# Kernel optimization log

Measured on AMD Instinct MI355X. Metric: run time of the kernel, lower is better.

## Reference

```python
import jax, jax.numpy as jnp
import numpy as np

N_NODES = 100000


def gcn_conv(x, src, dst, W, b, n):
    # x: [N, F_in]; src/dst: [E+N] (self-loops already appended)
    h = x @ W  # [N, F_out]
    deg = jax.ops.segment_sum(jnp.ones_like(dst, dtype=h.dtype), dst, num_segments=n)
    dinv = jnp.where(deg > 0, jax.lax.rsqrt(deg), 0.0)
    norm = dinv[src] * dinv[dst]  # [E+N]
    msgs = h[src] * norm[:, None]  # gather + scale
    out = jax.ops.segment_sum(msgs, dst, num_segments=n)  # scatter-add at dst
    return out + b


def setup_inputs() -> dict:
    key = jax.random.key(0)
    k1, k2, k3, ke = jax.random.split(key, 4)
    d = 64
    x = jax.random.normal(k1, (N_NODES, d), dtype=jnp.float32)
    edge_index = jax.random.randint(ke, (2, 1000000), 0, N_NODES, dtype=jnp.int64)
    s = 1.0 / np.sqrt(d)
    W1 = jax.random.normal(k2, (d, d), dtype=jnp.float32) * s
    b1 = jnp.zeros((d,), dtype=jnp.float32)
    W2 = jax.random.normal(k3, (d, d), dtype=jnp.float32) * s
    b2 = jnp.zeros((d,), dtype=jnp.float32)
    return {"x": x, "edge_index": edge_index, "W1": W1, "b1": b1, "W2": W2, "b2": b2}


def reference(x, edge_index, W1, b1, W2, b2):
    n = x.shape[0]
    loops = jnp.arange(n, dtype=edge_index.dtype)
    src = jnp.concatenate([edge_index[0], loops])
    dst = jnp.concatenate([edge_index[1], loops])
    h = gcn_conv(x, src, dst, W1, b1, n)
    h = jax.nn.relu(h)
    out = gcn_conv(h, src, dst, W2, b2, n)
    return out
```

## Files before the change

kernel.cpp:

```cpp
#include <hip/hip_runtime.h>

#define F 64
#define NCH 256

typedef __attribute__((ext_vector_type(8))) short bf16x8;
typedef __attribute__((ext_vector_type(4))) float f32x4;

static __device__ __forceinline__ unsigned short f2bf(float f) {
    unsigned u = __float_as_uint(f);
    return (unsigned short)((u + 0x7fffu + ((u >> 16) & 1u)) >> 16);
}
static __device__ __forceinline__ float bflo(unsigned u) { return __uint_as_float(u << 16); }
static __device__ __forceinline__ float bfhi(unsigned u) { return __uint_as_float(u & 0xffff0000u); }

__global__ __launch_bounds__(256) void k_fused0(const int* __restrict__ dst,
                                                int* __restrict__ histM,
                                                const float* __restrict__ W1,
                                                const float* __restrict__ W2,
                                                unsigned short* __restrict__ W2t,
                                                const float* __restrict__ X,
                                                unsigned short* __restrict__ hs1,
                                                int E, int chunk, int NB, int N) {
    __shared__ int h[512];
    __shared__ unsigned short Wl[64 * 72];
    __shared__ unsigned short Xs[64 * 72];
    const int t = threadIdx.x;
    const int b = blockIdx.x;

    if (b < NCH) {
        for (int i = t; i < NB; i += 256) h[i] = 0;
        __syncthreads();
        const int lo = b * chunk;
        const int hi = min(E, lo + chunk);
        for (int e = lo + t; e < hi; e += 256) {
            atomicAdd(&h[dst[e] >> 8], 1);
        }
        __syncthreads();
        for (int i = t; i < NB; i += 256) histM[i * NCH + b] = h[i];
        return;
    }
    if (b == NCH) {
#pragma unroll
        for (int i = 0; i < 16; ++i) {
            int e = t + i * 256;
            int n = e >> 6, k = e & 63;
            W2t[e] = f2bf(W2[k * 64 + n]);
        }
        return;
    }

    const int row0 = (b - NCH - 1) * 64;
#pragma unroll
    for (int i = 0; i < 16; ++i) {
        int e = t + i * 256;
        int n = e >> 6, k = e & 63;
        Wl[n * 72 + k] = f2bf(W1[k * 64 + n]);
    }
#pragma unroll
    for (int i = 0; i < 4; ++i) {
        int idx = t + i * 256;
        int r = idx >> 4, c = (idx & 15) * 4;
        int gr = row0 + r;
        float4 v = make_float4(0.f, 0.f, 0.f, 0.f);
        if (gr < N) v = *(const float4*)&X[(size_t)gr * F + c];
        unsigned p0 = (unsigned)f2bf(v.x) | ((unsigned)f2bf(v.y) << 16);
        unsigned p1 = (unsigned)f2bf(v.z) | ((unsigned)f2bf(v.w) << 16);
        *(uint2*)&Xs[r * 72 + c] = make_uint2(p0, p1);
    }
    __syncthreads();

    const int w    = t >> 6;
    const int lane = t & 63;
    const int l15  = lane & 15;
    const int quad = lane >> 4;

    bf16x8 bf[4][2];
#pragma unroll
    for (int ct = 0; ct < 4; ++ct)
#pragma unroll
        for (int kc = 0; kc < 2; ++kc)
            bf[ct][kc] = *(const bf16x8*)&Wl[(ct * 16 + l15) * 72 + kc * 32 + quad * 8];

    const int am = w * 16 + l15;
    bf16x8 af0 = *(const bf16x8*)&Xs[am * 72 + quad * 8];
    bf16x8 af1 = *(const bf16x8*)&Xs[am * 72 + 32 + quad * 8];

    f32x4 acc[4];
#pragma unroll
    for (int ct = 0; ct < 4; ++ct) {
        f32x4 z = {0.f, 0.f, 0.f, 0.f};
        z = __builtin_amdgcn_mfma_f32_16x16x32_bf16(af0, bf[ct][0], z, 0, 0, 0);
        z = __builtin_amdgcn_mfma_f32_16x16x32_bf16(af1, bf[ct][1], z, 0, 0, 0);
        acc[ct] = z;
    }

#pragma unroll
    for (int ct = 0; ct < 4; ++ct) {
#pragma unroll
        for (int r = 0; r < 4; ++r) {
            int row = row0 + w * 16 + quad * 4 + r;
            if (row < N)
                hs1[(size_t)row * F + ct * 16 + l15] = f2bf(acc[ct][r]);
        }
    }
}

__global__ __launch_bounds__(256) void s_part(const int* __restrict__ v,
                                              int* __restrict__ part, int M) {
    __shared__ int sd[256];
    const int t = threadIdx.x;
    const int base = blockIdx.x * 1024 + t * 4;
    int s = 0;
    if (base + 3 < M) {
        int4 d = *(const int4*)&v[base];
        s = d.x + d.y + d.z + d.w;
    } else {
#pragma unroll
        for (int j = 0; j < 4; ++j) if (base + j < M) s += v[base + j];
    }
    sd[t] = s;
    __syncthreads();
    for (int off = 128; off > 0; off >>= 1) {
        if (t < off) sd[t] += sd[t + off];
        __syncthreads();
    }
    if (t == 0) part[blockIdx.x] = sd[0];
}

__global__ __launch_bounds__(256) void s_scanp(int* __restrict__ part, int nb) {
    __shared__ int sums[256];
    const int t = threadIdx.x;
    int s = (t < nb) ? part[t] : 0;
    sums[t] = s;
    __syncthreads();
    for (int off = 1; off < 256; off <<= 1) {
        int v = (t >= off) ? sums[t - off] : 0;
        __syncthreads();
        sums[t] += v;
        __syncthreads();
    }
    if (t < nb) part[t] = sums[t] - s;
}

__global__ __launch_bounds__(256) void s_emit(int* __restrict__ v,
                                              const int* __restrict__ part, int M) {
    __shared__ int sums[256];
    const int t = threadIdx.x;
    const int base = blockIdx.x * 1024 + t * 4;
    int d0 = 0, d1 = 0, d2 = 0, d3 = 0;
    if (base + 3 < M) {
        int4 d = *(const int4*)&v[base];
        d0 = d.x; d1 = d.y; d2 = d.z; d3 = d.w;
    } else {
        if (base + 0 < M) d0 = v[base + 0];
        if (base + 1 < M) d1 = v[base + 1];
        if (base + 2 < M) d2 = v[base + 2];
        if (base + 3 < M) d3 = v[base + 3];
    }
    int tot = d0 + d1 + d2 + d3;
    sums[t] = tot;
    __syncthreads();
    for (int off = 1; off < 256; off <<= 1) {
        int x = (t >= off) ? sums[t - off] : 0;
        __syncthreads();
        sums[t] += x;
        __syncthreads();
    }
    int o0 = part[blockIdx.x] + sums[t] - tot;
    int e0 = o0, e1 = o0 + d0, e2 = e1 + d1, e3 = e2 + d2;
    if (base + 3 < M) {
        *(int4*)&v[base] = make_int4(e0, e1, e2, e3);
    } else {
        int ee[4] = {e0, e1, e2, e3};
        for (int j = 0; j < 4; ++j) if (base + j < M) v[base + j] = ee[j];
    }
}

__global__ __launch_bounds__(256) void k_scatter2(const int* __restrict__ src,
                                                  const int* __restrict__ dst,
                                                  const int* __restrict__ scanM,
                                                  int* __restrict__ ebuf,
                                                  int E, int chunk, int NB) {
    extern __shared__ int cur[];
    const int t = threadIdx.x;
    for (int i = t; i < NB; i += 256) cur[i] = scanM[i * NCH + blockIdx.x];
    __syncthreads();
    const int lo = blockIdx.x * chunk;
    const int hi = min(E, lo + chunk);
    for (int e = lo + t; e < hi; e += 256) {
        int s = src[e];
        int d = dst[e];
        int p = atomicAdd(&cur[d >> 8], 1);
        ebuf[p] = s | ((d & 255) << 17);
    }
}

__global__ __launch_bounds__(256) void k_csr(const int* __restrict__ ebuf,
                                             const int* __restrict__ scanM,
                                             int* __restrict__ rowptr,
                                             int* __restrict__ csr,
                                             float* __restrict__ dinv,
                                             int N, int E, int NB) {
    __shared__ int hist[256];
    __shared__ int scn[256];
    __shared__ int cur[256];
    const int t = threadIdx.x;
    const int bkt = blockIdx.x;
    const int beg = scanM[bkt * NCH];
    const int end = (bkt + 1 < NB) ? scanM[(bkt + 1) * NCH] : E;

    hist[t] = 0;
    __syncthreads();
    for (int e = beg + t; e < end; e += 256)
        atomicAdd(&hist[((unsigned)ebuf[e]) >> 17], 1);
    __syncthreads();

    scn[t] = hist[t];
    __syncthreads();
    for (int off = 1; off < 256; off <<= 1) {
        int v = (t >= off) ? scn[t - off] : 0;
        __syncthreads();
        scn[t] += v;
        __syncthreads();
    }

    {
        int excl = scn[t] - hist[t];
        int rp = beg + excl;
        int node = (bkt << 8) + t;
        cur[t] = rp;
        if (node < N) {
            rowptr[node] = rp;
            dinv[node] = rsqrtf((float)(hist[t] + 1));
        }
    }
    if (bkt == NB - 1 && t == 0) rowptr[N] = E;
    __syncthreads();

    for (int e = beg + t; e < end; e += 256) {
        int pk = ebuf[e];
        int p = atomicAdd(&cur[((unsigned)pk) >> 17], 1);
        csr[p] = pk & 0x1FFFF;
    }
}

__global__ __launch_bounds__(512) void k_aggmm(const unsigned short* __restrict__ hs1,
                                               const int* __restrict__ rowptr,
                                               const int* __restrict__ csr,
                                               const unsigned short* __restrict__ W2t,
                                               const float* __restrict__ b1,
                                               const float* __restrict__ dinv,
                                               unsigned short* __restrict__ hs2, int N) {
    __shared__ unsigned short Act[256 * 72];
    __shared__ unsigned short Wl[64 * 72];
    __shared__ float sdv[256];
    const int t = threadIdx.x;
    const int node0 = blockIdx.x << 8;

    {
        int idx = t;
        int n = idx >> 3, k = (idx & 7) * 8;
        *(uint4*)&Wl[n * 72 + k] = ((const uint4*)W2t)[idx];
    }

    const int lane = t & 7;
    const int nsub = t >> 3;
    const uint4* hsb = (const uint4*)hs1;
    float4 bb0 = *(const float4*)&b1[lane * 8];
    float4 bb1 = *(const float4*)&b1[lane * 8 + 4];

#pragma unroll
    for (int it = 0; it < 4; ++it) {
        int local = it * 64 + nsub;
        int node = node0 + local;
        float sc = 0.f;
        unsigned p0 = 0, p1 = 0, p2 = 0, p3 = 0;
        if (node < N) {
            int beg = rowptr[node];
            int end = rowptr[node + 1];
            sc = rsqrtf((float)(end - beg + 1));
            float a0, a1, a2, a3, a4, a5, a6, a7;
            {
                uint4 u = hsb[(size_t)node * 8 + lane];
                a0 = sc * bflo(u.x); a1 = sc * bfhi(u.x);
                a2 = sc * bflo(u.y); a3 = sc * bfhi(u.y);
                a4 = sc * bflo(u.z); a5 = sc * bfhi(u.z);
                a6 = sc * bflo(u.w); a7 = sc * bfhi(u.w);
            }
            for (int base = beg; base < end; base += 16) {
                int i0 = base + lane;
                int i1 = base + 8 + lane;
                int x0 = (i0 < end) ? csr[i0] : 0;
                int x1 = (i1 < end) ? csr[i1] : 0;
                uint4 r[16];
                float dv[16];
#pragma unroll
                for (int k = 0; k < 8; ++k) {
                    int s = __shfl(x0, k, 8);
                    r[k] = hsb[(size_t)s * 8 + lane];
                    dv[k] = dinv[s];
                }
#pragma unroll
                for (int k = 0; k < 8; ++k) {
                    int s = __shfl(x1, k, 8);
                    r[8 + k] = hsb[(size_t)s * 8 + lane];
                    dv[8 + k] = dinv[s];
                }
                int cnt = min(16, end - base);
#pragma unroll
                for (int k = 0; k < 16; ++k) {
                    if (k < cnt) {
                        uint4 u = r[k];
                        float w = dv[k];
                        a0 = fmaf(bflo(u.x), w, a0); a1 = fmaf(bfhi(u.x), w, a1);
                        a2 = fmaf(bflo(u.y), w, a2); a3 = fmaf(bfhi(u.y), w, a3);
                        a4 = fmaf(bflo(u.z), w, a4); a5 = fmaf(bfhi(u.z), w, a5);
                        a6 = fmaf(bflo(u.w), w, a6); a7 = fmaf(bfhi(u.w), w, a7);
                    }
                }
            }
            float o0 = fmaxf(a0 * sc + bb0.x, 0.f), o1 = fmaxf(a1 * sc + bb0.y, 0.f);
            float o2 = fmaxf(a2 * sc + bb0.z, 0.f), o3 = fmaxf(a3 * sc + bb0.w, 0.f);
            float o4 = fmaxf(a4 * sc + bb1.x, 0.f), o5 = fmaxf(a5 * sc + bb1.y, 0.f);
            float o6 = fmaxf(a6 * sc + bb1.z, 0.f), o7 = fmaxf(a7 * sc + bb1.w, 0.f);
            p0 = (unsigned)f2bf(o0) | ((unsigned)f2bf(o1) << 16);
            p1 = (unsigned)f2bf(o2) | ((unsigned)f2bf(o3) << 16);
            p2 = (unsigned)f2bf(o4) | ((unsigned)f2bf(o5) << 16);
            p3 = (unsigned)f2bf(o6) | ((unsigned)f2bf(o7) << 16);
        }
        *(uint4*)&Act[local * 72 + lane * 8] = make_uint4(p0, p1, p2, p3);
        if (lane == 0) sdv[local] = sc;
    }
    __syncthreads();

    const int w    = t >> 6;
    const int l    = t & 63;
    const int l15  = l & 15;
    const int quad = l >> 4;

    bf16x8 bf[4][2];
#pragma unroll
    for (int nt = 0; nt < 4; ++nt)
#pragma unroll
        for (int kc = 0; kc < 2; ++kc)
            bf[nt][kc] = *(const bf16x8*)&Wl[(nt * 16 + l15) * 72 + kc * 32 + quad * 8];

#pragma unroll
    for (int mt = 0; mt < 2; ++mt) {
        int m0 = w * 32 + mt * 16;
        bf16x8 af0 = *(const bf16x8*)&Act[(m0 + l15) * 72 + quad * 8];
        bf16x8 af1 = *(const bf16x8*)&Act[(m0 + l15) * 72 + 32 + quad * 8];
#pragma unroll
        for (int nt = 0; nt < 4; ++nt) {
            f32x4 z = {0.f, 0.f, 0.f, 0.f};
            z = __builtin_amdgcn_mfma_f32_16x16x32_bf16(af0, bf[nt][0], z, 0, 0, 0);
            z = __builtin_amdgcn_mfma_f32_16x16x32_bf16(af1, bf[nt][1], z, 0, 0, 0);
#pragma unroll
            for (int r = 0; r < 4; ++r) {
                int row = m0 + quad * 4 + r;
                int node = node0 + row;
                if (node < N)
                    hs2[((size_t)nt * N + node) * 16 + l15] = f2bf(z[r] * sdv[row]);
            }
        }
    }
}

__global__ __launch_bounds__(256) void k_agg2(const unsigned short* __restrict__ hs2,
                                              const int* __restrict__ rowptr,
                                              const int* __restrict__ csr,
                                              const float* __restrict__ dinv,
                                              const float* __restrict__ b,
                                              float* __restrict__ out, int N) {
    const int slice = blockIdx.x & 3;
    const int chunk = blockIdx.x >> 2;
    const int t = threadIdx.x;
    const int node = chunk * 64 + (t >> 2);
    const int lane = t & 3;
    if (node >= N) return;
    const int beg = rowptr[node];
    const int end = rowptr[node + 1];
    const unsigned short* hp = hs2 + (size_t)slice * N * 16;

    float a[16];
#pragma unroll
    for (int j = 0; j < 16; ++j) a[j] = 0.f;

    int e = beg + lane;
    int i0 = (e < end) ? csr[e] : -1;
    int i1 = (e + 4 < end) ? csr[e + 4] : -1;
    while (i0 >= 0) {
        int i2 = (e + 8  < end) ? csr[e + 8]  : -1;
        int i3 = (e + 12 < end) ? csr[e + 12] : -1;
        {
            const uint4* p = (const uint4*)(hp + (size_t)i0 * 16);
            uint4 u0 = p[0];
            uint4 u1 = p[1];
            a[0] += bflo(u0.x); a[1] += bfhi(u0.x);
            a[2] += bflo(u0.y); a[3] += bfhi(u0.y);
            a[4] += bflo(u0.z); a[5] += bfhi(u0.z);
            a[6] += bflo(u0.w); a[7] += bfhi(u0.w);
            a[8]  += bflo(u1.x); a[9]  += bfhi(u1.x);
            a[10] += bflo(u1.y); a[11] += bfhi(u1.y);
            a[12] += bflo(u1.z); a[13] += bfhi(u1.z);
            a[14] += bflo(u1.w); a[15] += bfhi(u1.w);
        }
        if (i1 >= 0) {
            const uint4* p = (const uint4*)(hp + (size_t)i1 * 16);
            uint4 u0 = p[0];
            uint4 u1 = p[1];
            a[0] += bflo(u0.x); a[1] += bfhi(u0.x);
            a[2] += bflo(u0.y); a[3] += bfhi(u0.y);
            a[4] += bflo(u0.z); a[5] += bfhi(u0.z);
            a[6] += bflo(u0.w); a[7] += bfhi(u0.w);
            a[8]  += bflo(u1.x); a[9]  += bfhi(u1.x);
            a[10] += bflo(u1.y); a[11] += bfhi(u1.y);
            a[12] += bflo(u1.z); a[13] += bfhi(u1.z);
            a[14] += bflo(u1.w); a[15] += bfhi(u1.w);
        }
        i0 = i2;
        i1 = i3;
        e += 8;
    }

    float h[8];
#pragma unroll
    for (int k = 0; k < 8; ++k) {
        float lo = a[k]     + __shfl_xor(a[k], 2, 4);
        float hi = a[k + 8] + __shfl_xor(a[k + 8], 2, 4);
        h[k] = (lane & 2) ? hi : lo;
    }
    float v[4];
#pragma unroll
    for (int k = 0; k < 4; ++k) {
        float lo = h[k]     + __shfl_xor(h[k], 1, 4);
        float hi = h[k + 4] + __shfl_xor(h[k + 4], 1, 4);
        v[k] = (lane & 1) ? hi : lo;
    }

    const float sc = dinv[node];
    const int j0 = lane * 4;
    uint2 sv = *(const uint2*)(hp + (size_t)node * 16 + j0);
    float s0 = bflo(sv.x), s1 = bfhi(sv.x), s2 = bflo(sv.y), s3 = bfhi(sv.y);
    float4 bb = *(const float4*)&b[slice * 16 + j0];
    float4 o = make_float4((v[0] + s0) * sc + bb.x,
                           (v[1] + s1) * sc + bb.y,
                           (v[2] + s2) * sc + bb.z,
                           (v[3] + s3) * sc + bb.w);
    *(float4*)&out[(size_t)node * F + slice * 16 + j0] = o;
}

extern "C" void kernel_launch(void* const* d_in, const int* in_sizes, int n_in,
                              void* d_out, int out_size, void* d_ws, size_t ws_size,
                              hipStream_t stream) {
    const float* x  = (const float*)d_in[0];
    const int*   ei = (const int*)d_in[1];
    const float* W1 = (const float*)d_in[2];
    const float* b1 = (const float*)d_in[3];
    const float* W2 = (const float*)d_in[4];
    const float* b2 = (const float*)d_in[5];
    float* out = (float*)d_out;

    const int N = in_sizes[0] / F;
    const int E = in_sizes[1] / 2;
    const int* src = ei;
    const int* dst = ei + E;

    const int NB = (N + 255) >> 8;
    const int chunk = (E + NCH - 1) / NCH;
    const int M  = NB * NCH;
    const int Mp = ((M + 1023) / 1024) * 1024;
    const int nb2 = Mp / 1024;

    char* ws = (char*)d_ws;
    size_t a = 0;
    unsigned short* W2t = (unsigned short*)(ws + a); a += (4096 * 2 + 255) & ~(size_t)255;
    float* dinv   = (float*)(ws + a); a += ((size_t)N * 4 + 255) & ~(size_t)255;
    int*   part2  = (int*)(ws + a);   a += ((size_t)nb2 * 4 + 255) & ~(size_t)255;
    int*   rowptr = (int*)(ws + a);   a += ((size_t)(N + 1) * 4 + 255) & ~(size_t)255;
    int*   histM  = (int*)(ws + a);   a += ((size_t)Mp * 4 + 255) & ~(size_t)255;
    int*   ebuf   = (int*)(ws + a);   a += ((size_t)E * 4 + 255) & ~(size_t)255;
    int*   csr    = (int*)(ws + a);   a += ((size_t)E * 4 + 255) & ~(size_t)255;
    unsigned short* hs1 = (unsigned short*)(ws + a); a += ((size_t)N * F * 2 + 255) & ~(size_t)255;
    unsigned short* hs2 = (unsigned short*)(ws + a);

    const size_t ldsNB = (size_t)NB * 4;
    const int gGemm = (N + 63) / 64;
    const int gAgg2 = ((N + 63) / 64) * 4;

    k_fused0<<<NCH + 1 + gGemm, 256, 0, stream>>>(dst, histM, W1, W2, W2t, x, hs1,
                                                  E, chunk, NB, N);
    s_part<<<nb2, 256, 0, stream>>>(histM, part2, M);
    s_scanp<<<1, 256, 0, stream>>>(part2, nb2);
    s_emit<<<nb2, 256, 0, stream>>>(histM, part2, M);
    k_scatter2<<<NCH, 256, ldsNB, stream>>>(src, dst, histM, ebuf, E, chunk, NB);
    k_csr<<<NB, 256, 0, stream>>>(ebuf, histM, rowptr, csr, dinv, N, E, NB);

    k_aggmm<<<NB, 512, 0, stream>>>(hs1, rowptr, csr, W2t, b1, dinv, hs2, N);
    k_agg2<<<gAgg2, 256, 0, stream>>>(hs2, rowptr, csr, dinv, b2, out, N);
}
```

Before: 193.4 us.

## Pre-scale layer-1 features by dinv in CSR kernel and fold scan launch

Source-side normalization is now applied once per node: k_csr multiplies each hs1 row by its dinv and writes it back in bf16. k_aggmm then drops the per-edge dinv gather and multiply and just sums neighbor rows. The standalone partial-scan kernel is also removed, and each emit block reduces the preceding partials itself, saving one launch. The cost is an extra read-modify-write of hs1 plus one more bf16 rounding of the scaled features.

```diff
diff --git a/kernel.cpp b/kernel.cpp
--- a/kernel.cpp
+++ b/kernel.cpp
@@ -127,26 +127,22 @@
     if (t == 0) part[blockIdx.x] = sd[0];
 }
 
-__global__ __launch_bounds__(256) void s_scanp(int* __restrict__ part, int nb) {
+__global__ __launch_bounds__(256) void s_emit2(int* __restrict__ v,
+                                               const int* __restrict__ part, int M) {
     __shared__ int sums[256];
-    const int t = threadIdx.x;
-    int s = (t < nb) ? part[t] : 0;
-    sums[t] = s;
-    __syncthreads();
-    for (int off = 1; off < 256; off <<= 1) {
-        int v = (t >= off) ? sums[t - off] : 0;
-        __syncthreads();
-        sums[t] += v;
-        __syncthreads();
-    }
-    if (t < nb) part[t] = sums[t] - s;
-}
-
-__global__ __launch_bounds__(256) void s_emit(int* __restrict__ v,
-                                              const int* __restrict__ part, int M) {
-    __shared__ int sums[256];
-    const int t = threadIdx.x;
-    const int base = blockIdx.x * 1024 + t * 4;
+    __shared__ int red[256];
+    const int t = threadIdx.x;
+    const int b = blockIdx.x;
+
+    red[t] = (t < b) ? part[t] : 0;
+    __syncthreads();
+    for (int off = 128; off > 0; off >>= 1) {
+        if (t < off) red[t] += red[t + off];
+        __syncthreads();
+    }
+    const int pref = red[0];
+
+    const int base = b * 1024 + t * 4;
     int d0 = 0, d1 = 0, d2 = 0, d3 = 0;
     if (base + 3 < M) {
         int4 d = *(const int4*)&v[base];
@@ -166,7 +162,7 @@
         sums[t] += x;
         __syncthreads();
     }
-    int o0 = part[blockIdx.x] + sums[t] - tot;
+    int o0 = pref + sums[t] - tot;
     int e0 = o0, e1 = o0 + d0, e2 = e1 + d1, e3 = e2 + d2;
     if (base + 3 < M) {
         *(int4*)&v[base] = make_int4(e0, e1, e2, e3);
@@ -200,6 +196,7 @@
                                              int* __restrict__ rowptr,
                                              int* __restrict__ csr,
                                              float* __restrict__ dinv,
+                                             unsigned short* __restrict__ hs1,
                                              int N, int E, int NB) {
     __shared__ int hist[256];
     __shared__ int scn[256];
@@ -224,17 +221,32 @@
         __syncthreads();
     }
 
+    const int node = (bkt << 8) + t;
+    float sc = 0.f;
     {
         int excl = scn[t] - hist[t];
         int rp = beg + excl;
-        int node = (bkt << 8) + t;
         cur[t] = rp;
         if (node < N) {
             rowptr[node] = rp;
-            dinv[node] = rsqrtf((float)(hist[t] + 1));
+            sc = rsqrtf((float)(hist[t] + 1));
+            dinv[node] = sc;
         }
     }
     if (bkt == NB - 1 && t == 0) rowptr[N] = E;
+
+    if (node < N) {
+        uint4* rowp = (uint4*)(hs1 + (size_t)node * F);
+#pragma unroll
+        for (int j = 0; j < 8; ++j) {
+            uint4 u = rowp[j];
+            u.x = (unsigned)f2bf(bflo(u.x) * sc) | ((unsigned)f2bf(bfhi(u.x) * sc) << 16);
+            u.y = (unsigned)f2bf(bflo(u.y) * sc) | ((unsigned)f2bf(bfhi(u.y) * sc) << 16);
+            u.z = (unsigned)f2bf(bflo(u.z) * sc) | ((unsigned)f2bf(bfhi(u.z) * sc) << 16);
+            u.w = (unsigned)f2bf(bflo(u.w) * sc) | ((unsigned)f2bf(bfhi(u.w) * sc) << 16);
+            rowp[j] = u;
+        }
+    }
     __syncthreads();
 
     for (int e = beg + t; e < end; e += 256) {
@@ -249,7 +261,6 @@
                                                const int* __restrict__ csr,
                                                const unsigned short* __restrict__ W2t,
                                                const float* __restrict__ b1,
-                                               const float* __restrict__ dinv,
                                                unsigned short* __restrict__ hs2, int N) {
     __shared__ unsigned short Act[256 * 72];
     __shared__ unsigned short Wl[64 * 72];
@@ -282,10 +293,10 @@
             float a0, a1, a2, a3, a4, a5, a6, a7;
             {
                 uint4 u = hsb[(size_t)node * 8 + lane];
-                a0 = sc * bflo(u.x); a1 = sc * bfhi(u.x);
-                a2 = sc * bflo(u.y); a3 = sc * bfhi(u.y);
-                a4 = sc * bflo(u.z); a5 = sc * bfhi(u.z);
-                a6 = sc * bflo(u.w); a7 = sc * bfhi(u.w);
+                a0 = bflo(u.x); a1 = bfhi(u.x);
+                a2 = bflo(u.y); a3 = bfhi(u.y);
+                a4 = bflo(u.z); a5 = bfhi(u.z);
+                a6 = bflo(u.w); a7 = bfhi(u.w);
             }
             for (int base = beg; base < end; base += 16) {
                 int i0 = base + lane;
@@ -293,29 +304,25 @@
                 int x0 = (i0 < end) ? csr[i0] : 0;
                 int x1 = (i1 < end) ? csr[i1] : 0;
                 uint4 r[16];
-                float dv[16];
 #pragma unroll
                 for (int k = 0; k < 8; ++k) {
                     int s = __shfl(x0, k, 8);
                     r[k] = hsb[(size_t)s * 8 + lane];
-                    dv[k] = dinv[s];
                 }
 #pragma unroll
                 for (int k = 0; k < 8; ++k) {
                     int s = __shfl(x1, k, 8);
                     r[8 + k] = hsb[(size_t)s * 8 + lane];
-                    dv[8 + k] = dinv[s];
                 }
                 int cnt = min(16, end - base);
 #pragma unroll
                 for (int k = 0; k < 16; ++k) {
                     if (k < cnt) {
                         uint4 u = r[k];
-                        float w = dv[k];
-                        a0 = fmaf(bflo(u.x), w, a0); a1 = fmaf(bfhi(u.x), w, a1);
-                        a2 = fmaf(bflo(u.y), w, a2); a3 = fmaf(bfhi(u.y), w, a3);
-                        a4 = fmaf(bflo(u.z), w, a4); a5 = fmaf(bfhi(u.z), w, a5);
-                        a6 = fmaf(bflo(u.w), w, a6); a7 = fmaf(bfhi(u.w), w, a7);
+                        a0 += bflo(u.x); a1 += bfhi(u.x);
+                        a2 += bflo(u.y); a3 += bfhi(u.y);
+                        a4 += bflo(u.z); a5 += bfhi(u.z);
+                        a6 += bflo(u.w); a7 += bfhi(u.w);
                     }
                 }
             }
@@ -491,11 +498,9 @@
     k_fused0<<<NCH + 1 + gGemm, 256, 0, stream>>>(dst, histM, W1, W2, W2t, x, hs1,
                                                   E, chunk, NB, N);
     s_part<<<nb2, 256, 0, stream>>>(histM, part2, M);
-    s_scanp<<<1, 256, 0, stream>>>(part2, nb2);
-    s_emit<<<nb2, 256, 0, stream>>>(histM, part2, M);
+    s_emit2<<<nb2, 256, 0, stream>>>(histM, part2, M);
     k_scatter2<<<NCH, 256, ldsNB, stream>>>(src, dst, histM, ebuf, E, chunk, NB);
-    k_csr<<<NB, 256, 0, stream>>>(ebuf, histM, rowptr, csr, dinv, N, E, NB);
-
-    k_aggmm<<<NB, 512, 0, stream>>>(hs1, rowptr, csr, W2t, b1, dinv, hs2, N);
+    k_csr<<<NB, 256, 0, stream>>>(ebuf, histM, rowptr, csr, dinv, hs1, N, E, NB);
+    k_aggmm<<<NB, 512, 0, stream>>>(hs1, rowptr, csr, W2t, b1, hs2, N);
     k_agg2<<<gAgg2, 256, 0, stream>>>(hs2, rowptr, csr, dinv, b2, out, N);
 }
```

Result: faster. 188.5 us (-2.5%).
